# Performance work log

Measured on AMD Instinct MI355X. Metric: run time of the kernel, lower is better.

The kernel has to match this reference:

```python
import jax, jax.numpy as jnp
import numpy as np

N_NODES = 50000
N_EDGES = 800000
IN_CH = 128
HID = 64
MLP_HID = 128
EPS = 1e-5


def setup_inputs() -> dict:
    key = jax.random.key(0)
    ks = iter(jax.random.split(key, 32))
    d = {}
    d['x'] = jax.random.normal(next(ks), (N_NODES, IN_CH), dtype=jnp.float32)
    d['edge_index'] = jax.random.randint(next(ks), (2, N_EDGES), 0, N_NODES, dtype=jnp.int64)

    def lin(k, out_c, in_c, scale=None):
        s = scale if scale is not None else 1.0 / np.sqrt(in_c)
        return jax.random.uniform(k, (out_c, in_c), jnp.float32, -s, s)

    # layer 0: in->hid, with residual linear
    d['Wl0'] = lin(next(ks), HID, IN_CH); d['bl0'] = jnp.zeros((HID,), jnp.float32)
    d['Wr0'] = lin(next(ks), HID, IN_CH)
    d['g0'] = jnp.ones((HID,), jnp.float32); d['be0'] = jnp.zeros((HID,), jnp.float32)
    d['rW0'] = lin(next(ks), HID, IN_CH); d['rb0'] = jnp.zeros((HID,), jnp.float32)
    # layers 1,2: hid->hid, identity residual
    for i in (1, 2):
        d[f'Wl{i}'] = lin(next(ks), HID, HID); d[f'bl{i}'] = jnp.zeros((HID,), jnp.float32)
        d[f'Wr{i}'] = lin(next(ks), HID, HID)
        d[f'g{i}'] = jnp.ones((HID,), jnp.float32); d[f'be{i}'] = jnp.zeros((HID,), jnp.float32)
    # edge MLP: 2*HID -> MLP_HID -> MLP_HID -> 1
    d['W1'] = lin(next(ks), MLP_HID, 2 * HID); d['b1'] = jnp.zeros((MLP_HID,), jnp.float32)
    d['W2'] = lin(next(ks), MLP_HID, MLP_HID); d['b2'] = jnp.zeros((MLP_HID,), jnp.float32)
    d['W3'] = lin(next(ks), 1, MLP_HID); d['b3'] = jnp.zeros((1,), jnp.float32)
    return d


def _res_sage_layer(x, src, tgt, Wl, bl, Wr, g, be, rW=None, rb=None):
    # SAGEConv (mean aggr): out = lin_l(mean_{j in N(i)} x_j) + lin_r(x_i)
    msg = x[src]                                              # [E, C] gather
    agg = jax.ops.segment_sum(msg, tgt, num_segments=N_NODES)
    cnt = jax.ops.segment_sum(jnp.ones((msg.shape[0],), x.dtype), tgt, num_segments=N_NODES)
    mean = agg / jnp.maximum(cnt, 1.0)[:, None]
    out = mean @ Wl.T + bl + x @ Wr.T
    # BatchNorm (training-mode batch statistics, biased var)
    mu = out.mean(axis=0)
    var = out.var(axis=0)
    out = (out - mu) * jax.lax.rsqrt(var + EPS) * g + be
    out = jax.nn.relu(out)
    res = x @ rW.T + rb if rW is not None else x
    return out + res


def reference(x, edge_index, Wl0, bl0, Wr0, g0, be0, rW0, rb0,
              Wl1, bl1, Wr1, g1, be1, Wl2, bl2, Wr2, g2, be2,
              W1, b1, W2, b2, W3, b3):
    src, tgt = edge_index[0], edge_index[1]
    h = _res_sage_layer(x, src, tgt, Wl0, bl0, Wr0, g0, be0, rW0, rb0)
    h = _res_sage_layer(h, src, tgt, Wl1, bl1, Wr1, g1, be1)
    h = _res_sage_layer(h, src, tgt, Wl2, bl2, Wr2, g2, be2)
    edge_repr = jnp.concatenate([h[src], h[tgt]], axis=1)     # [E, 2*HID]
    z = jax.nn.relu(edge_repr @ W1.T + b1)                    # dropout: eval mode (identity)
    z = jax.nn.relu(z @ W2.T + b2)
    return z @ W3.T + b3                                      # [E, 1]
```

## Files before the change

### kernel.cpp

```cpp
#include <hip/hip_runtime.h>
#include <hip/hip_bf16.h>

#define NN 50000
#define NE 800000
#define HID 64
#define EPSV 1e-5f
#define NBLK 196

typedef __attribute__((ext_vector_type(8))) short bf16x8;
typedef __attribute__((ext_vector_type(4))) float f32x4;
typedef __attribute__((ext_vector_type(4))) int int4v;

__device__ __forceinline__ ushort f2b(float f) {
    union { __hip_bfloat16 b; ushort u; } c;
    c.b = __float2bfloat16(f);
    return c.u;
}
__device__ __forceinline__ float b2f(ushort u) {
    return __uint_as_float(((unsigned int)u) << 16);
}

__global__ void prep_all_kernel(
    const float* __restrict__ W1, const float* __restrict__ W2,
    const float* __restrict__ Wl0, const float* __restrict__ Wr0, const float* __restrict__ rW0,
    const float* __restrict__ Wl1, const float* __restrict__ Wr1,
    const float* __restrict__ Wl2, const float* __restrict__ Wr2,
    ushort* __restrict__ W1b, ushort* __restrict__ W2b,
    ushort* __restrict__ wnb, int* __restrict__ icnt, float* __restrict__ bnbuf)
{
    int i = blockIdx.x * 256 + threadIdx.x;
    if      (i < 16384)  W1b[i] = f2b(W1[i]);
    else if (i < 32768)  W2b[i - 16384] = f2b(W2[i - 16384]);
    else if (i < 40960)  wnb[i - 32768] = f2b(Wl0[i - 32768]);
    else if (i < 49152)  wnb[i - 32768] = f2b(Wr0[i - 40960]);
    else if (i < 57344)  wnb[i - 32768] = f2b(rW0[i - 49152]);
    else if (i < 61440)  wnb[i - 32768] = f2b(Wl1[i - 57344]);
    else if (i < 65536)  wnb[i - 32768] = f2b(Wr1[i - 61440]);
    else if (i < 69632)  wnb[i - 32768] = f2b(Wl2[i - 65536]);
    else if (i < 73728)  wnb[i - 32768] = f2b(Wr2[i - 69632]);
    else if (i < 123728) icnt[i - 73728] = 0;
    else if (i < 124112) bnbuf[i - 123728] = 0.f;
}

__global__ void count_kernel(const int* __restrict__ tgt, int* __restrict__ icnt) {
    int e = blockIdx.x * 256 + threadIdx.x;
    if (e < NE) atomicAdd(&icnt[tgt[e]], 1);
}

__global__ void scanA_kernel(const int* __restrict__ icnt, int* __restrict__ off,
                             int* __restrict__ bsum) {
    __shared__ int s[256];
    const int t = threadIdx.x;
    const int i = blockIdx.x * 256 + t;
    int v = (i < NN) ? icnt[i] : 0;
    s[t] = v;
    __syncthreads();
    for (int d = 1; d < 256; d <<= 1) {
        int x = (t >= d) ? s[t - d] : 0;
        __syncthreads();
        s[t] += x;
        __syncthreads();
    }
    if (i < NN) off[i] = s[t];
    if (t == 255) bsum[blockIdx.x] = s[255];
}

__global__ void scanB_kernel(const int* __restrict__ icnt, const int* __restrict__ bsum,
                             int* __restrict__ off, int* __restrict__ woff) {
    __shared__ int red[256];
    const int t = threadIdx.x, bid = blockIdx.x;
    int s = 0;
    for (int j = t; j < bid; j += 256) s += bsum[j];
    red[t] = s;
    __syncthreads();
    for (int d = 128; d > 0; d >>= 1) {
        if (t < d) red[t] += red[t + d];
        __syncthreads();
    }
    const int bpre = red[0];
    const int i = bid * 256 + t;
    if (i < NN) {
        int e = off[i] - icnt[i] + bpre;
        off[i] = e;
        woff[i] = e;
        if (i == NN - 1) off[NN] = NE;
    }
}

__global__ void fill_kernel(const int* __restrict__ src, const int* __restrict__ tgt,
                            int* __restrict__ woff, int* __restrict__ ebuf) {
    int e = blockIdx.x * 256 + threadIdx.x;
    if (e < NE) {
        int p = atomicAdd(&woff[tgt[e]], 1);
        ebuf[p] = src[e];
    }
}

__global__ __launch_bounds__(256) void proj0_mfma_kernel(
    const float* __restrict__ x,
    const ushort* __restrict__ w0, const ushort* __restrict__ w1,
    const ushort* __restrict__ w2,
    const float* __restrict__ bias1, const float* __restrict__ bias2,
    ushort* __restrict__ xb, float* __restrict__ pre, float* __restrict__ res)
{
    __shared__ ushort xt[128 * 128];
    __shared__ float sC[128][65];
    const int tid = threadIdx.x;
    const int wv = tid >> 6, lane = tid & 63;
    const int l15 = lane & 15, l4 = lane >> 4;
    const int n0 = blockIdx.x * 128;

    {
        const int rloc = tid >> 1;
        int row = n0 + rloc; if (row > NN - 1) row = NN - 1;
        const int c0 = (tid & 1) * 64;
        #pragma unroll
        for (int gq = 0; gq < 8; gq++) {
            int c = c0 + gq * 8;
            float4 f0 = *(const float4*)&x[(long)row * 128 + c];
            float4 f1 = *(const float4*)&x[(long)row * 128 + c + 4];
            union { ushort u[8]; int4v v; } a;
            a.u[0] = f2b(f0.x); a.u[1] = f2b(f0.y); a.u[2] = f2b(f0.z); a.u[3] = f2b(f0.w);
            a.u[4] = f2b(f1.x); a.u[5] = f2b(f1.y); a.u[6] = f2b(f1.z); a.u[7] = f2b(f1.w);
            int byte = rloc * 256 + ((c * 2) ^ ((rloc & 7) << 4));
            *(int4v*)((char*)xt + byte) = a.v;
        }
    }
    __syncthreads();

    for (int seg = 0; seg < 3; seg++) {
        const ushort* W = (seg == 0) ? w0 : ((seg == 1) ? w1 : w2);
        bf16x8 wf[4][4];
        #pragma unroll
        for (int n = 0; n < 4; n++)
            #pragma unroll
            for (int ks = 0; ks < 4; ks++)
                wf[n][ks] = *(const bf16x8*)&W[(n * 16 + l15) * 128 + ks * 32 + l4 * 8];

        f32x4 acc[2][4];
        #pragma unroll
        for (int m = 0; m < 2; m++)
            #pragma unroll
            for (int n = 0; n < 4; n++)
                acc[m][n] = (f32x4){0.f, 0.f, 0.f, 0.f};

        #pragma unroll
        for (int m = 0; m < 2; m++) {
            const int row = wv * 32 + m * 16 + l15;
            #pragma unroll
            for (int ks = 0; ks < 4; ks++) {
                int byte = row * 256 + ((ks * 64 + l4 * 16) ^ ((row & 7) << 4));
                bf16x8 a = *(const bf16x8*)((const char*)xt + byte);
                #pragma unroll
                for (int n = 0; n < 4; n++)
                    acc[m][n] = __builtin_amdgcn_mfma_f32_16x16x32_bf16(a, wf[n][ks], acc[m][n], 0, 0, 0);
            }
        }
        #pragma unroll
        for (int m = 0; m < 2; m++)
            #pragma unroll
            for (int n = 0; n < 4; n++)
                #pragma unroll
                for (int r = 0; r < 4; r++)
                    sC[wv * 32 + m * 16 + l4 * 4 + r][n * 16 + l15] = acc[m][n][r];
        __syncthreads();

        const int r = tid >> 1, ch = (tid & 1) * 32;
        const int node = n0 + r;
        if (node < NN) {
            if (seg == 0) {
                #pragma unroll
                for (int gq = 0; gq < 4; gq++) {
                    union { ushort u[8]; int4v v; } pk;
                    #pragma unroll
                    for (int j = 0; j < 8; j++)
                        pk.u[j] = f2b(sC[r][ch + gq * 8 + j]);
                    *(int4v*)&xb[(long)node * 64 + ch + gq * 8] = pk.v;
                }
            } else {
                float* O = (seg == 1) ? pre : res;
                const float* bp = (seg == 1) ? bias1 : bias2;
                #pragma unroll
                for (int gq = 0; gq < 8; gq++) {
                    int c = ch + gq * 4;
                    float4 v = make_float4(sC[r][c + 0] + bp[c + 0], sC[r][c + 1] + bp[c + 1],
                                           sC[r][c + 2] + bp[c + 2], sC[r][c + 3] + bp[c + 3]);
                    *(float4*)&O[(long)node * 64 + c] = v;
                }
            }
        }
        __syncthreads();
    }
}

__global__ __launch_bounds__(256) void gather_bn_kernel(
    const int* __restrict__ off, const int* __restrict__ ebuf,
    const ushort* __restrict__ xb,
    float* __restrict__ vbase,
    float* __restrict__ bnsum, float* __restrict__ bnsq)
{
    __shared__ float r1[4][64], r2[4][64];
    const int lane = threadIdx.x & 63;
    const int wid = __builtin_amdgcn_readfirstlane(threadIdx.x >> 6);
    const int eslot = lane >> 3;
    const int cg = lane & 7;
    float s8[8], q8[8];
    #pragma unroll
    for (int j = 0; j < 8; j++) { s8[j] = 0.f; q8[j] = 0.f; }

    for (int n = blockIdx.x * 4 + wid; n < NN; n += gridDim.x * 4) {
        const int a = off[n], b = off[n + 1];
        float acc[8];
        #pragma unroll
        for (int j = 0; j < 8; j++) acc[j] = 0.f;
        for (int p = a + eslot; p < b; p += 8) {
            int sidx = ebuf[p];
            union { int4v v; ushort u[8]; } cv;
            cv.v = *(const int4v*)&xb[(long)sidx * 64 + cg * 8];
            #pragma unroll
            for (int j = 0; j < 8; j++) acc[j] += b2f(cv.u[j]);
        }
        #pragma unroll
        for (int m = 8; m <= 32; m <<= 1)
            #pragma unroll
            for (int j = 0; j < 8; j++)
                acc[j] += __shfl_xor(acc[j], m);
        if (eslot == 0) {
            const float inv_deg = 1.0f / fmaxf((float)(b - a), 1.f);
            float4 p0 = *(const float4*)&vbase[(long)n * 64 + cg * 8];
            float4 p1 = *(const float4*)&vbase[(long)n * 64 + cg * 8 + 4];
            float v[8];
            v[0] = acc[0] * inv_deg + p0.x; v[1] = acc[1] * inv_deg + p0.y;
            v[2] = acc[2] * inv_deg + p0.z; v[3] = acc[3] * inv_deg + p0.w;
            v[4] = acc[4] * inv_deg + p1.x; v[5] = acc[5] * inv_deg + p1.y;
            v[6] = acc[6] * inv_deg + p1.z; v[7] = acc[7] * inv_deg + p1.w;
            *(float4*)&vbase[(long)n * 64 + cg * 8]     = make_float4(v[0], v[1], v[2], v[3]);
            *(float4*)&vbase[(long)n * 64 + cg * 8 + 4] = make_float4(v[4], v[5], v[6], v[7]);
            #pragma unroll
            for (int j = 0; j < 8; j++) { s8[j] += v[j]; q8[j] += v[j] * v[j]; }
        }
    }
    if (eslot == 0) {
        #pragma unroll
        for (int j = 0; j < 8; j++) {
            r1[wid][cg * 8 + j] = s8[j];
            r2[wid][cg * 8 + j] = q8[j];
        }
    }
    __syncthreads();
    if (threadIdx.x < 64) {
        float s = r1[0][lane] + r1[1][lane] + r1[2][lane] + r1[3][lane];
        float q = r2[0][lane] + r2[1][lane] + r2[2][lane] + r2[3][lane];
        atomicAdd(&bnsum[lane], s);
        atomicAdd(&bnsq[lane], q);
    }
}

__global__ __launch_bounds__(256) void apply_proj_kernel(
    const float* __restrict__ vIn,
    const float* __restrict__ resb,
    const float* __restrict__ bnsum, const float* __restrict__ bnsq,
    const float* __restrict__ g, const float* __restrict__ be,
    float* __restrict__ hout,
    const ushort* __restrict__ Wl, const ushort* __restrict__ Wr,
    const float* __restrict__ bias,
    ushort* __restrict__ xb, float* __restrict__ preOut)
{
    __shared__ float scs[64], shs[64];
    __shared__ ushort tile[128 * 72];
    __shared__ float sC[128][65];
    const int tid = threadIdx.x;
    const int n0 = blockIdx.x * 128;
    const int wv = tid >> 6, lane = tid & 63;
    const int l15 = lane & 15, l4 = lane >> 4;

    if (tid < 64) {
        const float inv_n = 1.0f / (float)NN;
        float mu = bnsum[tid] * inv_n;
        float var = bnsq[tid] * inv_n - mu * mu;
        float rstd = rsqrtf(var + EPSV);
        float sc = g[tid] * rstd;
        scs[tid] = sc;
        shs[tid] = be[tid] - mu * sc;
    }
    __syncthreads();

    {
        const int rloc = tid >> 1;
        const int n = n0 + rloc;
        const int ch = (tid & 1) * 32;
        if (n < NN) {
            #pragma unroll
            for (int gq = 0; gq < 4; gq++) {
                int c = ch + gq * 8;
                float4 v0 = *(const float4*)&vIn[(long)n * 64 + c];
                float4 v1 = *(const float4*)&vIn[(long)n * 64 + c + 4];
                float4 r0 = *(const float4*)&resb[(long)n * 64 + c];
                float4 r1 = *(const float4*)&resb[(long)n * 64 + c + 4];
                float o[8];
                o[0] = fmaxf(fmaf(v0.x, scs[c + 0], shs[c + 0]), 0.f) + r0.x;
                o[1] = fmaxf(fmaf(v0.y, scs[c + 1], shs[c + 1]), 0.f) + r0.y;
                o[2] = fmaxf(fmaf(v0.z, scs[c + 2], shs[c + 2]), 0.f) + r0.z;
                o[3] = fmaxf(fmaf(v0.w, scs[c + 3], shs[c + 3]), 0.f) + r0.w;
                o[4] = fmaxf(fmaf(v1.x, scs[c + 4], shs[c + 4]), 0.f) + r1.x;
                o[5] = fmaxf(fmaf(v1.y, scs[c + 5], shs[c + 5]), 0.f) + r1.y;
                o[6] = fmaxf(fmaf(v1.z, scs[c + 6], shs[c + 6]), 0.f) + r1.z;
                o[7] = fmaxf(fmaf(v1.w, scs[c + 7], shs[c + 7]), 0.f) + r1.w;
                *(float4*)&hout[(long)n * 64 + c]     = make_float4(o[0], o[1], o[2], o[3]);
                *(float4*)&hout[(long)n * 64 + c + 4] = make_float4(o[4], o[5], o[6], o[7]);
                union { ushort u[8]; int4v v; } pk;
                #pragma unroll
                for (int j = 0; j < 8; j++) pk.u[j] = f2b(o[j]);
                int byte = rloc * 144 + ((c * 2) ^ ((rloc & 7) << 4));
                *(int4v*)((char*)tile + byte) = pk.v;
            }
        }
    }
    __syncthreads();

    for (int seg = 0; seg < 2; seg++) {
        const ushort* W = seg ? Wr : Wl;
        bf16x8 wf[4][2];
        #pragma unroll
        for (int n = 0; n < 4; n++)
            #pragma unroll
            for (int ks = 0; ks < 2; ks++)
                wf[n][ks] = *(const bf16x8*)&W[(n * 16 + l15) * 64 + ks * 32 + l4 * 8];

        f32x4 acc[2][4];
        #pragma unroll
        for (int m = 0; m < 2; m++)
            #pragma unroll
            for (int n = 0; n < 4; n++)
                acc[m][n] = (f32x4){0.f, 0.f, 0.f, 0.f};

        #pragma unroll
        for (int m = 0; m < 2; m++) {
            const int row = wv * 32 + m * 16 + l15;
            #pragma unroll
            for (int ks = 0; ks < 2; ks++) {
                int byte = row * 144 + ((((ks * 32 + l4 * 8) * 2)) ^ ((row & 7) << 4));
                bf16x8 a = *(const bf16x8*)((const char*)tile + byte);
                #pragma unroll
                for (int n = 0; n < 4; n++)
                    acc[m][n] = __builtin_amdgcn_mfma_f32_16x16x32_bf16(a, wf[n][ks], acc[m][n], 0, 0, 0);
            }
        }
        #pragma unroll
        for (int m = 0; m < 2; m++)
            #pragma unroll
            for (int n = 0; n < 4; n++)
                #pragma unroll
                for (int r = 0; r < 4; r++)
                    sC[wv * 32 + m * 16 + l4 * 4 + r][n * 16 + l15] = acc[m][n][r];
        __syncthreads();

        const int r = tid >> 1, ch = (tid & 1) * 32;
        const int node = n0 + r;
        if (node < NN) {
            if (seg == 0) {
                #pragma unroll
                for (int gq = 0; gq < 4; gq++) {
                    union { ushort u[8]; int4v v; } pk;
                    #pragma unroll
                    for (int j = 0; j < 8; j++)
                        pk.u[j] = f2b(sC[r][ch + gq * 8 + j]);
                    *(int4v*)&xb[(long)node * 64 + ch + gq * 8] = pk.v;
                }
            } else {
                #pragma unroll
                for (int gq = 0; gq < 8; gq++) {
                    int c = ch + gq * 4;
                    float4 v = make_float4(sC[r][c + 0] + bias[c + 0], sC[r][c + 1] + bias[c + 1],
                                           sC[r][c + 2] + bias[c + 2], sC[r][c + 3] + bias[c + 3]);
                    *(float4*)&preOut[(long)node * 64 + c] = v;
                }
            }
        }
        __syncthreads();
    }
}

__global__ void apply_final_kernel(const float* __restrict__ vIn,
                                   const float* __restrict__ resb,
                                   const float* __restrict__ bnsum, const float* __restrict__ bnsq,
                                   const float* __restrict__ g, const float* __restrict__ be,
                                   ushort* __restrict__ hb)
{
    const float inv_n = 1.0f / (float)NN;
    const int stride = gridDim.x * 256;
    for (int i = blockIdx.x * 256 + threadIdx.x; i < NN * 16; i += stride) {
        int n = i >> 4;
        int c0 = (i & 15) * 4;
        float sc[4], sh[4];
        #pragma unroll
        for (int j = 0; j < 4; j++) {
            int c = c0 + j;
            float mu = bnsum[c] * inv_n;
            float var = bnsq[c] * inv_n - mu * mu;
            float rstd = rsqrtf(var + EPSV);
            sc[j] = g[c] * rstd;
            sh[j] = be[c] - mu * sc[j];
        }
        float4 v = *(const float4*)&vIn[(long)n * 64 + c0];
        float4 r = *(const float4*)&resb[(long)n * 64 + c0];
        union { ushort u[4]; uint2 v2; } p;
        p.u[0] = f2b(fmaxf(fmaf(v.x, sc[0], sh[0]), 0.f) + r.x);
        p.u[1] = f2b(fmaxf(fmaf(v.y, sc[1], sh[1]), 0.f) + r.y);
        p.u[2] = f2b(fmaxf(fmaf(v.z, sc[2], sh[2]), 0.f) + r.z);
        p.u[3] = f2b(fmaxf(fmaf(v.w, sc[3], sh[3]), 0.f) + r.w);
        *(uint2*)&hb[(long)n * 64 + c0] = p.v2;
    }
}

#define NSTRIP 25000
#define EMG 256
#define ZSTR 136

#define GATHER(ss)                                                        \
    do {                                                                  \
        int e0g = (ss) * 32;                                              \
        _Pragma("unroll")                                                 \
        for (int m = 0; m < 2; m++) {                                     \
            int e = e0g + m * 16 + l15;                                   \
            const ushort* hs = hb + (long)src[e] * 64;                    \
            const ushort* ht = hb + (long)tgt[e] * 64;                    \
            ga[m][0] = *(const bf16x8*)&hs[l4 * 8];                       \
            ga[m][1] = *(const bf16x8*)&hs[32 + l4 * 8];                  \
            ga[m][2] = *(const bf16x8*)&ht[l4 * 8];                       \
            ga[m][3] = *(const bf16x8*)&ht[32 + l4 * 8];                  \
        }                                                                 \
    } while (0)

__global__ __launch_bounds__(512) void edge_mlp_wave_kernel(
    const ushort* __restrict__ hb,
    const int* __restrict__ src, const int* __restrict__ tgt,
    const ushort* __restrict__ W1b, const ushort* __restrict__ W2b,
    const float* __restrict__ b1, const float* __restrict__ b2,
    const float* __restrict__ W3, const float* __restrict__ b3,
    float* __restrict__ out)
{
    __shared__ ushort wlds[32768];
    __shared__ ushort z1[8][32 * ZSTR];

    const int tid = threadIdx.x;
    const int wid = tid >> 6, lane = tid & 63;
    const int l15 = lane & 15, l4 = lane >> 4;

    for (int c = tid; c < 4096; c += 512) {
        int layer = c >> 11, oc = (c >> 4) & 127, kc = c & 15;
        const ushort* Wsrc = layer ? W2b : W1b;
        int4v v = *(const int4v*)&Wsrc[oc * 128 + kc * 8];
        int byte = layer * 32768 + oc * 256 + ((kc * 16) ^ ((oc & 7) << 4));
        *(int4v*)((char*)wlds + byte) = v;
    }

    float4 b1q[8];
    float b2v[8], w3v[8];
    #pragma unroll
    for (int n = 0; n < 8; n++) {
        b1q[n] = *(const float4*)&b1[n * 16 + l4 * 4];
        int oc = n * 16 + l15;
        b2v[n] = b2[oc]; w3v[n] = W3[oc];
    }
    const float b3v = b3[0];

    const int bid = blockIdx.x;
    const int q = NSTRIP / EMG, r = NSTRIP % EMG;
    const int t0 = bid * q + (bid < r ? bid : r);
    const int nt = q + (bid < r ? 1 : 0);
    ushort* zw = z1[wid];

    bf16x8 ga[2][4];
    if (wid < nt) GATHER(t0 + wid);
    __syncthreads();

    for (int j = wid; j < nt; j += 8) {
        const int e0 = (t0 + j) * 32;

        f32x4 acc[2][8];
        #pragma unroll
        for (int m = 0; m < 2; m++)
            #pragma unroll
            for (int n = 0; n < 8; n++)
                acc[m][n] = (f32x4){b1q[n].x, b1q[n].y, b1q[n].z, b1q[n].w};
        #pragma unroll
        for (int ks = 0; ks < 4; ks++) {
            bf16x8 wf[8];
            #pragma unroll
            for (int n = 0; n < 8; n++) {
                int oc = n * 16 + l15;
                int byte = oc * 256 + (((ks * 4 + l4) * 16) ^ ((oc & 7) << 4));
                wf[n] = *(const bf16x8*)((const char*)wlds + byte);
            }
            #pragma unroll
            for (int m = 0; m < 2; m++)
                #pragma unroll
                for (int n = 0; n < 8; n++)
                    acc[m][n] = __builtin_amdgcn_mfma_f32_16x16x32_bf16(wf[n], ga[m][ks], acc[m][n], 0, 0, 0);
        }
        #pragma unroll
        for (int m = 0; m < 2; m++)
            #pragma unroll
            for (int n = 0; n < 8; n++) {
                union { ushort u[4]; uint2 d; } pk;
                #pragma unroll
                for (int rr = 0; rr < 4; rr++)
                    pk.u[rr] = f2b(fmaxf(acc[m][n][rr], 0.f));
                *(uint2*)&zw[(m * 16 + l15) * ZSTR + n * 16 + l4 * 4] = pk.d;
            }

        if (j + 8 < nt) GATHER(t0 + j + 8);

        f32x4 acc2[2][8];
        #pragma unroll
        for (int m = 0; m < 2; m++)
            #pragma unroll
            for (int n = 0; n < 8; n++)
                acc2[m][n] = (f32x4){b2v[n], b2v[n], b2v[n], b2v[n]};
        #pragma unroll
        for (int ks = 0; ks < 4; ks++) {
            bf16x8 wf[8];
            #pragma unroll
            for (int n = 0; n < 8; n++) {
                int oc = n * 16 + l15;
                int byte = 32768 + oc * 256 + (((ks * 4 + l4) * 16) ^ ((oc & 7) << 4));
                wf[n] = *(const bf16x8*)((const char*)wlds + byte);
            }
            bf16x8 a2[2];
            #pragma unroll
            for (int m = 0; m < 2; m++)
                a2[m] = *(const bf16x8*)&zw[(m * 16 + l15) * ZSTR + ks * 32 + l4 * 8];
            #pragma unroll
            for (int m = 0; m < 2; m++)
                #pragma unroll
                for (int n = 0; n < 8; n++)
                    acc2[m][n] = __builtin_amdgcn_mfma_f32_16x16x32_bf16(a2[m], wf[n], acc2[m][n], 0, 0, 0);
        }

        #pragma unroll
        for (int m = 0; m < 2; m++) {
            float sv[4];
            #pragma unroll
            for (int rr = 0; rr < 4; rr++) {
                float s = 0.f;
                #pragma unroll
                for (int n = 0; n < 8; n++)
                    s = fmaf(fmaxf(acc2[m][n][rr], 0.f), w3v[n], s);
                s += __shfl_xor(s, 1);
                s += __shfl_xor(s, 2);
                s += __shfl_xor(s, 4);
                s += __shfl_xor(s, 8);
                sv[rr] = s + b3v;
            }
            if (l15 == 0)
                *(float4*)&out[e0 + m * 16 + l4 * 4] =
                    make_float4(sv[0], sv[1], sv[2], sv[3]);
        }
    }
}

extern "C" void kernel_launch(void* const* d_in, const int* in_sizes, int n_in,
                              void* d_out, int out_size, void* d_ws, size_t ws_size,
                              hipStream_t stream)
{
    const float* x   = (const float*)d_in[0];
    const int*   ei  = (const int*)d_in[1];
    const int* src = ei;
    const int* tgt = ei + NE;
    const float* Wl0 = (const float*)d_in[2];
    const float* bl0 = (const float*)d_in[3];
    const float* Wr0 = (const float*)d_in[4];
    const float* g0  = (const float*)d_in[5];
    const float* be0 = (const float*)d_in[6];
    const float* rW0 = (const float*)d_in[7];
    const float* rb0 = (const float*)d_in[8];
    const float* Wl1 = (const float*)d_in[9];
    const float* bl1 = (const float*)d_in[10];
    const float* Wr1 = (const float*)d_in[11];
    const float* g1  = (const float*)d_in[12];
    const float* be1 = (const float*)d_in[13];
    const float* Wl2 = (const float*)d_in[14];
    const float* bl2 = (const float*)d_in[15];
    const float* Wr2 = (const float*)d_in[16];
    const float* g2  = (const float*)d_in[17];
    const float* be2 = (const float*)d_in[18];
    const float* W1  = (const float*)d_in[19];
    const float* b1  = (const float*)d_in[20];
    const float* W2  = (const float*)d_in[21];
    const float* b2  = (const float*)d_in[22];
    const float* W3  = (const float*)d_in[23];
    const float* b3  = (const float*)d_in[24];
    float* out = (float*)d_out;

    float* ws = (float*)d_ws;
    float*  pre  = ws;
    float*  res  = ws + 3200000;
    float*  hbuf = ws + 6400000;
    ushort* xb   = (ushort*)(ws + 9600256);
    ushort* hb   = (ushort*)(ws + 11200256);
    ushort* W1b  = (ushort*)(ws + 12800256);
    ushort* W2b  = W1b + 16384;
    int*    icnt = (int*)(ws + 12816640);
    int*    off  = icnt + 50000;
    int*    woff = off + 50001;
    int*    ebuf = woff + 50000;
    int*    bsum = ebuf + 800000;
    ushort* wnb  = (ushort*)(ws + 13766912);
    ushort* Wl0b = wnb;
    ushort* Wr0b = wnb + 8192;
    ushort* rW0b = wnb + 16384;
    ushort* Wl1b = wnb + 24576;
    ushort* Wr1b = wnb + 28672;
    ushort* Wl2b = wnb + 32768;
    ushort* Wr2b = wnb + 36864;
    float*  bn   = ws + 13787392;
    float*  bnsum0 = bn,       *bnsq0 = bn + 64;
    float*  bnsum1 = bn + 128, *bnsq1 = bn + 192;
    float*  bnsum2 = bn + 256, *bnsq2 = bn + 320;

    prep_all_kernel<<<485, 256, 0, stream>>>(W1, W2, Wl0, Wr0, rW0, Wl1, Wr1, Wl2, Wr2,
                                             W1b, W2b, wnb, icnt, bn);
    count_kernel<<<NE / 256, 256, 0, stream>>>(tgt, icnt);
    scanA_kernel<<<NBLK, 256, 0, stream>>>(icnt, off, bsum);
    scanB_kernel<<<NBLK, 256, 0, stream>>>(icnt, bsum, off, woff);
    fill_kernel<<<NE / 256, 256, 0, stream>>>(src, tgt, woff, ebuf);

    proj0_mfma_kernel<<<391, 256, 0, stream>>>(x, Wl0b, Wr0b, rW0b, bl0, rb0, xb, pre, res);
    gather_bn_kernel<<<1024, 256, 0, stream>>>(off, ebuf, xb, pre, bnsum0, bnsq0);

    apply_proj_kernel<<<391, 256, 0, stream>>>(pre, res, bnsum0, bnsq0, g0, be0,
                                               hbuf, Wl1b, Wr1b, bl1, xb, pre);
    gather_bn_kernel<<<1024, 256, 0, stream>>>(off, ebuf, xb, pre, bnsum1, bnsq1);

    apply_proj_kernel<<<391, 256, 0, stream>>>(pre, hbuf, bnsum1, bnsq1, g1, be1,
                                               hbuf, Wl2b, Wr2b, bl2, xb, pre);
    gather_bn_kernel<<<1024, 256, 0, stream>>>(off, ebuf, xb, pre, bnsum2, bnsq2);

    apply_final_kernel<<<1024, 256, 0, stream>>>(pre, hbuf, bnsum2, bnsq2, g2, be2, hb);

    edge_mlp_wave_kernel<<<EMG, 512, 0, stream>>>(hb, src, tgt, W1b, W2b, b1, b2, W3, b3, out);
}
```

Before: 389.0 us.

## Pass edge-MLP hidden activations between layers via cross-lane shuffles instead of LDS

The edge MLP kernel no longer stages the first hidden layer's bf16 activations in a per-wave LDS buffer. Results are packed into registers and rearranged with __shfl so they match the A-operand layout of the second MFMA layer. Processing the two 16-edge halves one after another halves the accumulator arrays, which lowers register pressure. Dropping the z1 LDS buffer frees shared memory, and the grid size doubles from 256 to 512 blocks. In exchange the code issues many extra ds_bpermute shuffles and the next-tile gather prefetch moves later in the loop.

```diff
diff --git a/kernel.cpp b/kernel.cpp
--- a/kernel.cpp
+++ b/kernel.cpp
@@ -18,6 +18,9 @@
 }
 __device__ __forceinline__ float b2f(ushort u) {
     return __uint_as_float(((unsigned int)u) << 16);
+}
+__device__ __forceinline__ unsigned int pk2(float a, float b) {
+    return (unsigned int)f2b(a) | ((unsigned int)f2b(b) << 16);
 }
 
 __global__ void prep_all_kernel(
@@ -414,8 +417,7 @@
 }
 
 #define NSTRIP 25000
-#define EMG 256
-#define ZSTR 136
+#define EMG 512
 
 #define GATHER(ss)                                                        \
     do {                                                                  \
@@ -441,7 +443,6 @@
     float* __restrict__ out)
 {
     __shared__ ushort wlds[32768];
-    __shared__ ushort z1[8][32 * ZSTR];
 
     const int tid = threadIdx.x;
     const int wid = tid >> 6, lane = tid & 63;
@@ -469,84 +470,77 @@
     const int q = NSTRIP / EMG, r = NSTRIP % EMG;
     const int t0 = bid * q + (bid < r ? bid : r);
     const int nt = q + (bid < r ? 1 : 0);
-    ushort* zw = z1[wid];
 
     bf16x8 ga[2][4];
     if (wid < nt) GATHER(t0 + wid);
     __syncthreads();
 
+    const int slBase = l15 + ((l4 & 1) << 5);
+
     for (int j = wid; j < nt; j += 8) {
         const int e0 = (t0 + j) * 32;
 
-        f32x4 acc[2][8];
-        #pragma unroll
-        for (int m = 0; m < 2; m++)
+        #pragma unroll
+        for (int m = 0; m < 2; m++) {
+            f32x4 acc[8];
             #pragma unroll
             for (int n = 0; n < 8; n++)
-                acc[m][n] = (f32x4){b1q[n].x, b1q[n].y, b1q[n].z, b1q[n].w};
-        #pragma unroll
-        for (int ks = 0; ks < 4; ks++) {
-            bf16x8 wf[8];
+                acc[n] = (f32x4){b1q[n].x, b1q[n].y, b1q[n].z, b1q[n].w};
+            #pragma unroll
+            for (int ks = 0; ks < 4; ks++) {
+                bf16x8 wf[8];
+                #pragma unroll
+                for (int n = 0; n < 8; n++) {
+                    int oc = n * 16 + l15;
+                    int byte = oc * 256 + (((ks * 4 + l4) * 16) ^ ((oc & 7) << 4));
+                    wf[n] = *(const bf16x8*)((const char*)wlds + byte);
+                }
+                #pragma unroll
+                for (int n = 0; n < 8; n++)
+                    acc[n] = __builtin_amdgcn_mfma_f32_16x16x32_bf16(wf[n], ga[m][ks], acc[n], 0, 0, 0);
+            }
+            unsigned int zp[8][2];
             #pragma unroll
             for (int n = 0; n < 8; n++) {
-                int oc = n * 16 + l15;
-                int byte = oc * 256 + (((ks * 4 + l4) * 16) ^ ((oc & 7) << 4));
-                wf[n] = *(const bf16x8*)((const char*)wlds + byte);
-            }
-            #pragma unroll
-            for (int m = 0; m < 2; m++)
+                zp[n][0] = pk2(fmaxf(acc[n][0], 0.f), fmaxf(acc[n][1], 0.f));
+                zp[n][1] = pk2(fmaxf(acc[n][2], 0.f), fmaxf(acc[n][3], 0.f));
+            }
+
+            if (m == 1 && j + 8 < nt) GATHER(t0 + j + 8);
+
+            f32x4 acc2[8];
+            #pragma unroll
+            for (int n = 0; n < 8; n++)
+                acc2[n] = (f32x4){b2v[n], b2v[n], b2v[n], b2v[n]};
+            #pragma unroll
+            for (int ks = 0; ks < 4; ks++) {
+                union { unsigned int d[4]; bf16x8 v; } a2u;
+                #pragma unroll
+                for (int d = 0; d < 4; d++) {
+                    int sl = slBase + ((d >> 1) << 4);
+                    unsigned int vA = (unsigned int)__shfl((int)zp[2 * ks][d & 1], sl);
+                    unsigned int vB = (unsigned int)__shfl((int)zp[2 * ks + 1][d & 1], sl);
+                    a2u.d[d] = (l4 < 2) ? vA : vB;
+                }
+                bf16x8 wf[8];
+                #pragma unroll
+                for (int n = 0; n < 8; n++) {
+                    int oc = n * 16 + l15;
+                    int byte = 32768 + oc * 256 + (((ks * 4 + l4) * 16) ^ ((oc & 7) << 4));
+                    wf[n] = *(const bf16x8*)((const char*)wlds + byte);
+                }
                 #pragma unroll
                 for (int n = 0; n < 8; n++)
-                    acc[m][n] = __builtin_amdgcn_mfma_f32_16x16x32_bf16(wf[n], ga[m][ks], acc[m][n], 0, 0, 0);
-        }
-        #pragma unroll
-        for (int m = 0; m < 2; m++)
-            #pragma unroll
-            for (int n = 0; n < 8; n++) {
-                union { ushort u[4]; uint2 d; } pk;
-                #pragma unroll
-                for (int rr = 0; rr < 4; rr++)
-                    pk.u[rr] = f2b(fmaxf(acc[m][n][rr], 0.f));
-                *(uint2*)&zw[(m * 16 + l15) * ZSTR + n * 16 + l4 * 4] = pk.d;
-            }
-
-        if (j + 8 < nt) GATHER(t0 + j + 8);
-
-        f32x4 acc2[2][8];
-        #pragma unroll
-        for (int m = 0; m < 2; m++)
-            #pragma unroll
-            for (int n = 0; n < 8; n++)
-                acc2[m][n] = (f32x4){b2v[n], b2v[n], b2v[n], b2v[n]};
-        #pragma unroll
-        for (int ks = 0; ks < 4; ks++) {
-            bf16x8 wf[8];
-            #pragma unroll
-            for (int n = 0; n < 8; n++) {
-                int oc = n * 16 + l15;
-                int byte = 32768 + oc * 256 + (((ks * 4 + l4) * 16) ^ ((oc & 7) << 4));
-                wf[n] = *(const bf16x8*)((const char*)wlds + byte);
-            }
-            bf16x8 a2[2];
-            #pragma unroll
-            for (int m = 0; m < 2; m++)
-                a2[m] = *(const bf16x8*)&zw[(m * 16 + l15) * ZSTR + ks * 32 + l4 * 8];
-            #pragma unroll
-            for (int m = 0; m < 2; m++)
-                #pragma unroll
-                for (int n = 0; n < 8; n++)
-                    acc2[m][n] = __builtin_amdgcn_mfma_f32_16x16x32_bf16(a2[m], wf[n], acc2[m][n], 0, 0, 0);
-        }
-
-        #pragma unroll
-        for (int m = 0; m < 2; m++) {
+                    acc2[n] = __builtin_amdgcn_mfma_f32_16x16x32_bf16(a2u.v, wf[n], acc2[n], 0, 0, 0);
+            }
+
             float sv[4];
             #pragma unroll
             for (int rr = 0; rr < 4; rr++) {
                 float s = 0.f;
                 #pragma unroll
                 for (int n = 0; n < 8; n++)
-                    s = fmaf(fmaxf(acc2[m][n][rr], 0.f), w3v[n], s);
+                    s = fmaf(fmaxf(acc2[n][rr], 0.f), w3v[n], s);
                 s += __shfl_xor(s, 1);
                 s += __shfl_xor(s, 2);
                 s += __shfl_xor(s, 4);
```

Measured after the change: 712.4 us. +83.1%, slower.
